# Optimization experiments

Measured on AMD Instinct MI355X. Metric: run time of the kernel, lower is better.

Reference implementation:

```python
import jax, jax.numpy as jnp
import numpy as np

K = 20          # neighbors per point (knn k=20)
BN_EPS = 1e-5   # torch BatchNorm1d default eps
NEG_SLOPE = 0.2 # LeakyReLU negative_slope


def setup_inputs() -> dict:
    key = jax.random.key(0)
    k1, k2 = jax.random.split(key)
    B, N, H = 8, 4096, 64
    pcd = jax.random.normal(k1, (B, N, 3), dtype=jnp.float32)
    W = jax.random.normal(k2, (6, H), dtype=jnp.float32) * (1.0 / np.sqrt(6.0))
    b = jnp.zeros((H,), dtype=jnp.float32)
    gamma = jnp.ones((H,), dtype=jnp.float32)
    beta = jnp.zeros((H,), dtype=jnp.float32)
    return {"pcd": pcd, "W": W, "b": b, "gamma": gamma, "beta": beta}


def reference(pcd, W, b, gamma, beta):
    # pcd: [B, N, 3]
    # --- kNN graph construction (per cloud, includes self like torch_geometric knn) ---
    sq = jnp.sum(pcd * pcd, axis=-1)                          # [B, N]
    # squared distances: |xi|^2 + |xj|^2 - 2 xi.xj  -> [B, N, N]
    d2 = sq[:, :, None] + sq[:, None, :] - 2.0 * jnp.einsum("bnd,bmd->bnm", pcd, pcd)
    _, idx = jax.lax.top_k(-d2, K)                            # idx: [B, N, K] neighbor indices

    # --- edge feature gather: concat(x_j, x_i - x_j) ---
    nbr = jax.vmap(lambda p, i: p[i])(pcd, idx)               # [B, N, K, 3]
    feat = jnp.concatenate([nbr, pcd[:, :, None, :] - nbr], axis=-1)  # [B, N, K, 6]

    # --- shared MLP: Linear(6,64) + BatchNorm1d(64, training stats) + LeakyReLU(0.2) ---
    h = jnp.einsum("bnkf,fh->bnkh", feat, W) + b              # [B, N, K, 64]
    mean = jnp.mean(h, axis=(0, 1, 2))
    var = jnp.mean((h - mean) ** 2, axis=(0, 1, 2))           # biased var (BN train mode)
    h = (h - mean) * jax.lax.rsqrt(var + BN_EPS) * gamma + beta
    h = jnp.where(h >= 0, h, NEG_SLOPE * h)

    # --- max-pool over the K edges of each point (max_pool_x per cluster) ---
    return jnp.max(h, axis=2)                                 # [B, N, 64]
```

## Files before the change

kernel.cpp:

```cpp
#include <hip/hip_runtime.h>
#include <math.h>

#define KNN 20
#define NPTS 4096
#define BATCH 8
#define P_TOT (BATCH * NPTS)
#define QPW 8
#define WPB 8
#define QPB (QPW * WPB)
#define NBLK (P_TOT / QPB)
#define BPB (NPTS / QPB)
#define BN_EPS 1e-5
#define NEG_SLOPE 0.2f

#define FO_CLOUD 0
#define FO_PART  131072
#define FO_PART2 196608
#define FO_AB    655360
#define FO_W2    655488
#define FO_BIG   655936

__global__ __launch_bounds__(256) void pack_kernel(const float* __restrict__ pcd,
                                                   float4* __restrict__ cloud) {
    int i = blockIdx.x * 256 + threadIdx.x;
    float x = pcd[3 * i], y = pcd[3 * i + 1], z = pcd[3 * i + 2];
    float sq = __fadd_rn(__fadd_rn(__fmul_rn(x, x), __fmul_rn(y, y)), __fmul_rn(z, z));
    cloud[i] = make_float4(x, y, z, sq);
}

#define DIST(C) ({ \
    float dot_ = __fadd_rn(__fadd_rn(__fmul_rn(qx, (C).x), __fmul_rn(qy, (C).y)), \
                           __fmul_rn(qz, (C).z)); \
    fmaf(-2.0f, dot_, __fadd_rn(qs, (C).w)); })

#define RECOMP(G) { \
    float m1 = INFINITY, m2 = INFINITY; int s1 = 0, s2 = 0; \
    _Pragma("unroll") \
    for (int e = 0; e < 8; ++e) { \
        const int sl = (G) * 8 + e; \
        const float4 C = cl[sl * 64 + lane]; \
        float dd = DIST(C); \
        if ((mask >> sl) & 1ull) dd = INFINITY; \
        if (dd < m1) { m2 = m1; s2 = s1; m1 = dd; s1 = sl; } \
        else if (dd < m2) { m2 = dd; s2 = sl; } \
    } \
    gv1[G] = m1; gs1[G] = s1; gv2[G] = m2; gs2[G] = s2; }

#define PROMOTE(G) { \
    if (gv2[G] < INFINITY) { gv1[G] = gv2[G]; gs1[G] = gs2[G]; gv2[G] = INFINITY; } \
    else { RECOMP(G) } }

template <bool FAST>
__global__ __launch_bounds__(512, 2) void knn_kernel(const float4* __restrict__ cloud,
                                                     const float* __restrict__ W,
                                                     const float* __restrict__ bias,
                                                     float* __restrict__ partials,
                                                     float* __restrict__ rawmax,
                                                     float* __restrict__ rawmin,
                                                     int* __restrict__ idxo) {
    __shared__ float4 cl[NPTS];
    const int t = threadIdx.x;
    const int wave = t >> 6, lane = t & 63;
    const int bidx = blockIdx.x;
    const int batch = bidx / BPB;
    const int gbase = batch * NPTS;

#pragma unroll
    for (int it = 0; it < NPTS / 512; ++it)
        cl[it * 512 + t] = cloud[gbase + it * 512 + t];
    __syncthreads();

    const float wc3 = W[192 + lane], wc4 = W[256 + lane], wc5 = W[320 + lane];
    const float wd0 = W[lane] - wc3, wd1 = W[64 + lane] - wc4, wd2 = W[128 + lane] - wc5;
    const float bb = bias[lane];
    float se = 0.f, sqs = 0.f;

#pragma unroll 1
    for (int qi = 0; qi < QPW; ++qi) {
        const int q = (bidx % BPB) * QPB + wave * QPW + qi;
        const int gq = gbase + q;
        const float4 Q = cl[q];
        const float qx = Q.x, qy = Q.y, qz = Q.z, qs = Q.w;
        const float qoff = fmaf(wc3, qx, fmaf(wc4, qy, fmaf(wc5, qz, bb)));

        float gv1[8], gv2[8];
        int gs1[8], gs2[8];
#pragma unroll
        for (int g = 0; g < 8; ++g) { gv1[g] = INFINITY; gv2[g] = INFINITY; gs1[g] = 0; gs2[g] = 0; }
#pragma unroll
        for (int g = 0; g < 8; ++g) {
#pragma unroll
            for (int e = 0; e < 8; ++e) {
                const int j = g * 8 + e;
                const float4 C = cl[j * 64 + lane];
                const float dd = DIST(C);
                const bool c1 = dd < gv1[g];
                const bool c2 = dd < gv2[g];
                gv2[g] = c1 ? gv1[g] : (c2 ? dd : gv2[g]);
                gs2[g] = c1 ? gs1[g] : (c2 ? j : gs2[g]);
                gv1[g] = c1 ? dd : gv1[g];
                gs1[g] = c1 ? j : gs1[g];
            }
            __builtin_amdgcn_sched_barrier(0);
        }
        float dmin = gv1[0]; int bs = gs1[0];
#pragma unroll
        for (int g = 1; g < 8; ++g) if (gv1[g] < dmin) { dmin = gv1[g]; bs = gs1[g]; }
        int mmin = bs * 64 + lane;
        unsigned long long mask = 0ull;
        float hmax = -INFINITY, hmin = INFINITY;

#pragma unroll 1
        for (int p = 0; p < KNN; ++p) {
            float gmin = dmin;
#pragma unroll
            for (int off = 32; off; off >>= 1) gmin = fminf(gmin, __shfl_xor(gmin, off));
            unsigned long long bal = __ballot(dmin == gmin);
            int win;
            if (__popcll(bal) > 1) {
                int mv = (dmin == gmin) ? mmin : 0x7FFFFFFF;
#pragma unroll
                for (int off = 32; off; off >>= 1) mv = min(mv, __shfl_xor(mv, off));
                win = mv;
            } else {
                win = __shfl(mmin, __ffsll((unsigned long long)bal) - 1);
            }

            if (!FAST) { if (lane == 0) idxo[gq * KNN + p] = win; }

            const float4 C = cl[win];
            const float raw = fmaf(wd0, C.x, fmaf(wd1, C.y, fmaf(wd2, C.z, qoff)));
            se += raw;
            sqs = fmaf(raw, raw, sqs);
            hmax = fmaxf(hmax, raw);
            hmin = fminf(hmin, raw);

            if ((win & 63) == lane) {
                const int slot = win >> 6;
                mask |= (1ull << slot);
                switch (slot >> 3) {
                    case 0: PROMOTE(0); break;
                    case 1: PROMOTE(1); break;
                    case 2: PROMOTE(2); break;
                    case 3: PROMOTE(3); break;
                    case 4: PROMOTE(4); break;
                    case 5: PROMOTE(5); break;
                    case 6: PROMOTE(6); break;
                    default: PROMOTE(7); break;
                }
                float nv = gv1[0]; int ns = gs1[0];
#pragma unroll
                for (int g2 = 1; g2 < 8; ++g2) if (gv1[g2] < nv) { nv = gv1[g2]; ns = gs1[g2]; }
                dmin = nv; mmin = ns * 64 + lane;
            }
        }

        if (FAST) {
            rawmax[gq * 64 + lane] = hmax;
            rawmin[gq * 64 + lane] = hmin;
        }
    }

    __syncthreads();
    float* sred = (float*)cl;
    sred[wave * 128 + lane] = se;
    sred[wave * 128 + 64 + lane] = sqs;
    __syncthreads();
    if (t < 128) {
        float s = 0.f;
#pragma unroll
        for (int w = 0; w < WPB; ++w) s += sred[w * 128 + t];
        partials[bidx * 128 + t] = s;
    }
}

__global__ __launch_bounds__(128) void finA_kernel(const float* __restrict__ partials,
                                                   float* __restrict__ part2) {
    const int b = blockIdx.x, t = threadIdx.x;
    float s = 0.f;
#pragma unroll
    for (int i = 0; i < 8; ++i) s += partials[(b * 8 + i) * 128 + t];
    part2[b * 128 + t] = s;
}

__global__ __launch_bounds__(64) void finB_kernel(const float* __restrict__ part2,
                                                  const float* __restrict__ W,
                                                  const float* __restrict__ bias,
                                                  const float* __restrict__ gamma,
                                                  const float* __restrict__ beta,
                                                  float* __restrict__ ab,
                                                  float* __restrict__ w2) {
    const int c = threadIdx.x;
    double s0 = 0.0, s1 = 0.0, q0 = 0.0, q1 = 0.0;
    for (int i = 0; i < 64; i += 2) {
        s0 += (double)part2[i * 128 + c];
        q0 += (double)part2[i * 128 + 64 + c];
        s1 += (double)part2[(i + 1) * 128 + c];
        q1 += (double)part2[(i + 1) * 128 + 64 + c];
    }
    const double cnt = (double)P_TOT * KNN;
    double mean = (s0 + s1) / cnt;
    double var = (q0 + q1) / cnt - mean * mean;
    double a = (double)gamma[c] / sqrt(var + BN_EPS);
    float af = (float)a;
    float sh = (float)((double)beta[c] - mean * a);
    ab[c] = af;
    ab[64 + c] = sh;
#pragma unroll
    for (int f = 0; f < 6; ++f) w2[f * 64 + c] = W[f * 64 + c] * af;
    w2[384 + c] = fmaf(bias[c], af, sh);
}

__global__ __launch_bounds__(256) void final_kernel(const float* __restrict__ ab,
                                                    const float* __restrict__ rawmin,
                                                    float* __restrict__ out) {
    int i = blockIdx.x * 256 + threadIdx.x;
    int c = i & 63;
    float a = ab[c], sh = ab[64 + c];
    float va = fmaf(a, out[i], sh);
    float vb = fmaf(a, rawmin[i], sh);
    va = va >= 0.f ? va : NEG_SLOPE * va;
    vb = vb >= 0.f ? vb : NEG_SLOPE * vb;
    out[i] = fmaxf(va, vb);
}

__global__ __launch_bounds__(256) void out_kernel(const float4* __restrict__ cloud,
                                                  const int* __restrict__ idxo,
                                                  const float* __restrict__ w2,
                                                  float* __restrict__ out) {
    const int t = threadIdx.x, c = t & 63;
    const int gp = blockIdx.x * 4 + (t >> 6);
    const int gb = gp & ~(NPTS - 1);
    const float wc0 = w2[c], wc1 = w2[64 + c], wc2 = w2[128 + c];
    const float wc3 = w2[192 + c], wc4 = w2[256 + c], wc5 = w2[320 + c];
    const float bc = w2[384 + c];
    const float4 Q = cloud[gp];
    float vmax = -INFINITY;
    for (int k = 0; k < KNN; ++k) {
        const int m = idxo[gp * KNN + k];
        const float4 C = cloud[gb + m];
        float h = bc;
        h = fmaf(wc0, C.x, h);
        h = fmaf(wc1, C.y, h);
        h = fmaf(wc2, C.z, h);
        h = fmaf(wc3, Q.x - C.x, h);
        h = fmaf(wc4, Q.y - C.y, h);
        h = fmaf(wc5, Q.z - C.z, h);
        h = h >= 0.f ? h : NEG_SLOPE * h;
        vmax = fmaxf(vmax, h);
    }
    out[gp * 64 + c] = vmax;
}

extern "C" void kernel_launch(void* const* d_in, const int* in_sizes, int n_in,
                              void* d_out, int out_size, void* d_ws, size_t ws_size,
                              hipStream_t stream) {
    const float* pcd   = (const float*)d_in[0];
    const float* W     = (const float*)d_in[1];
    const float* bias  = (const float*)d_in[2];
    const float* gamma = (const float*)d_in[3];
    const float* beta  = (const float*)d_in[4];

    float* wsf = (float*)d_ws;
    float4* cloud   = (float4*)(wsf + FO_CLOUD);
    float* partials = wsf + FO_PART;
    float* part2    = wsf + FO_PART2;
    float* ab       = wsf + FO_AB;
    float* w2       = wsf + FO_W2;
    float* big      = wsf + FO_BIG;
    float* out      = (float*)d_out;

    const size_t need_fast = (size_t)FO_BIG * 4 + (size_t)P_TOT * 64 * 4 + 1024;
    const bool fast = ws_size >= need_fast;

    pack_kernel<<<P_TOT / 256, 256, 0, stream>>>(pcd, cloud);
    if (fast) {
        knn_kernel<true><<<NBLK, 512, 0, stream>>>(cloud, W, bias, partials, out, big, nullptr);
        finA_kernel<<<64, 128, 0, stream>>>(partials, part2);
        finB_kernel<<<1, 64, 0, stream>>>(part2, W, bias, gamma, beta, ab, w2);
        final_kernel<<<(P_TOT * 64) / 256, 256, 0, stream>>>(ab, big, out);
    } else {
        knn_kernel<false><<<NBLK, 512, 0, stream>>>(cloud, W, bias, partials, nullptr, nullptr, (int*)big);
        finA_kernel<<<64, 128, 0, stream>>>(partials, part2);
        finB_kernel<<<1, 64, 0, stream>>>(part2, W, bias, gamma, beta, ab, w2);
        out_kernel<<<P_TOT / 4, 256, 0, stream>>>(cloud, (int*)big, w2, out);
    }
}
```

Baseline: 217.4 us.

## Process two queries per wave and use DPP/swizzle wave reductions in kNN

The kNN kernel now handles two query points per wave iteration, so each LDS load of a candidate point feeds two distance computations and the two 20-step selection loops are interleaved for more instruction-level parallelism. The shuffle-based wave min-reductions are replaced with ds_swizzle plus a single bpermute, and winner broadcast uses readlane. The cost is doubled per-query register state (32 extra candidate slots), which may raise VGPR pressure under the 512x2 launch bounds and risk spills.

```diff
diff --git a/kernel.cpp b/kernel.cpp
--- a/kernel.cpp
+++ b/kernel.cpp
@@ -28,27 +28,81 @@
     cloud[i] = make_float4(x, y, z, sq);
 }
 
-#define DIST(C) ({ \
-    float dot_ = __fadd_rn(__fadd_rn(__fmul_rn(qx, (C).x), __fmul_rn(qy, (C).y)), \
-                           __fmul_rn(qz, (C).z)); \
-    fmaf(-2.0f, dot_, __fadd_rn(qs, (C).w)); })
-
-#define RECOMP(G) { \
-    float m1 = INFINITY, m2 = INFINITY; int s1 = 0, s2 = 0; \
-    _Pragma("unroll") \
-    for (int e = 0; e < 8; ++e) { \
-        const int sl = (G) * 8 + e; \
-        const float4 C = cl[sl * 64 + lane]; \
-        float dd = DIST(C); \
-        if ((mask >> sl) & 1ull) dd = INFINITY; \
-        if (dd < m1) { m2 = m1; s2 = s1; m1 = dd; s1 = sl; } \
-        else if (dd < m2) { m2 = dd; s2 = sl; } \
-    } \
-    gv1[G] = m1; gs1[G] = s1; gv2[G] = m2; gs2[G] = s2; }
-
-#define PROMOTE(G) { \
-    if (gv2[G] < INFINITY) { gv1[G] = gv2[G]; gs1[G] = gs2[G]; gv2[G] = INFINITY; } \
-    else { RECOMP(G) } }
+__device__ __forceinline__ float distf(float4 C, float qx, float qy, float qz, float qs) {
+    float dot_ = __fadd_rn(__fadd_rn(__fmul_rn(qx, C.x), __fmul_rn(qy, C.y)),
+                           __fmul_rn(qz, C.z));
+    return fmaf(-2.0f, dot_, __fadd_rn(qs, C.w));
+}
+
+__device__ __forceinline__ void upd2(float& v1, float& v2, int& s1, int& s2, float dd, int j) {
+    const bool c1 = dd < v1;
+    const bool c2 = dd < v2;
+    v2 = c1 ? v1 : (c2 ? dd : v2);
+    s2 = c1 ? s1 : (c2 ? j : s2);
+    v1 = c1 ? dd : v1;
+    s1 = c1 ? j : s1;
+}
+
+__device__ __forceinline__ float wmin_f(float v, int a32) {
+    v = fminf(v, __int_as_float(__builtin_amdgcn_ds_swizzle(__float_as_int(v), 0x041F)));
+    v = fminf(v, __int_as_float(__builtin_amdgcn_ds_swizzle(__float_as_int(v), 0x081F)));
+    v = fminf(v, __int_as_float(__builtin_amdgcn_ds_swizzle(__float_as_int(v), 0x101F)));
+    v = fminf(v, __int_as_float(__builtin_amdgcn_ds_swizzle(__float_as_int(v), 0x201F)));
+    v = fminf(v, __int_as_float(__builtin_amdgcn_ds_swizzle(__float_as_int(v), 0x401F)));
+    v = fminf(v, __int_as_float(__builtin_amdgcn_ds_bpermute(a32, __float_as_int(v))));
+    return v;
+}
+__device__ __forceinline__ int wmin_i(int v, int a32) {
+    v = min(v, __builtin_amdgcn_ds_swizzle(v, 0x041F));
+    v = min(v, __builtin_amdgcn_ds_swizzle(v, 0x081F));
+    v = min(v, __builtin_amdgcn_ds_swizzle(v, 0x101F));
+    v = min(v, __builtin_amdgcn_ds_swizzle(v, 0x201F));
+    v = min(v, __builtin_amdgcn_ds_swizzle(v, 0x401F));
+    v = min(v, __builtin_amdgcn_ds_bpermute(a32, v));
+    return v;
+}
+
+template <int G>
+__device__ __forceinline__ void prom(float (&gv1)[8], float (&gv2)[8], int (&gs1)[8], int (&gs2)[8],
+                                     unsigned long long mask, const float4* cl, int lane,
+                                     float qx, float qy, float qz, float qs) {
+    if (gv2[G] < INFINITY) {
+        gv1[G] = gv2[G]; gs1[G] = gs2[G]; gv2[G] = INFINITY;
+    } else {
+        float m1 = INFINITY, m2 = INFINITY; int s1 = 0, s2 = 0;
+#pragma unroll
+        for (int e = 0; e < 8; ++e) {
+            const int sl = G * 8 + e;
+            const float4 C = cl[sl * 64 + lane];
+            float dd = distf(C, qx, qy, qz, qs);
+            if ((mask >> sl) & 1ull) dd = INFINITY;
+            upd2(m1, m2, s1, s2, dd, sl);
+        }
+        gv1[G] = m1; gv2[G] = m2; gs1[G] = s1; gs2[G] = s2;
+    }
+}
+
+__device__ __forceinline__ void repair(float (&gv1)[8], float (&gv2)[8], int (&gs1)[8], int (&gs2)[8],
+                                       unsigned long long& mask, float& dmin, int& mmin,
+                                       int win, int lane, const float4* cl,
+                                       float qx, float qy, float qz, float qs) {
+    const int slot = win >> 6;
+    mask |= (1ull << slot);
+    switch (slot >> 3) {
+        case 0: prom<0>(gv1, gv2, gs1, gs2, mask, cl, lane, qx, qy, qz, qs); break;
+        case 1: prom<1>(gv1, gv2, gs1, gs2, mask, cl, lane, qx, qy, qz, qs); break;
+        case 2: prom<2>(gv1, gv2, gs1, gs2, mask, cl, lane, qx, qy, qz, qs); break;
+        case 3: prom<3>(gv1, gv2, gs1, gs2, mask, cl, lane, qx, qy, qz, qs); break;
+        case 4: prom<4>(gv1, gv2, gs1, gs2, mask, cl, lane, qx, qy, qz, qs); break;
+        case 5: prom<5>(gv1, gv2, gs1, gs2, mask, cl, lane, qx, qy, qz, qs); break;
+        case 6: prom<6>(gv1, gv2, gs1, gs2, mask, cl, lane, qx, qy, qz, qs); break;
+        default: prom<7>(gv1, gv2, gs1, gs2, mask, cl, lane, qx, qy, qz, qs); break;
+    }
+    float nv = gv1[0]; int ns = gs1[0];
+#pragma unroll
+    for (int g = 1; g < 8; ++g) if (gv1[g] < nv) { nv = gv1[g]; ns = gs1[g]; }
+    dmin = nv; mmin = ns * 64 + lane;
+}
 
 template <bool FAST>
 __global__ __launch_bounds__(512, 2) void knn_kernel(const float4* __restrict__ cloud,
@@ -61,6 +115,7 @@
     __shared__ float4 cl[NPTS];
     const int t = threadIdx.x;
     const int wave = t >> 6, lane = t & 63;
+    const int a32 = ((lane ^ 32) << 2);
     const int bidx = blockIdx.x;
     const int batch = bidx / BPB;
     const int gbase = batch * NPTS;
@@ -76,88 +131,95 @@
     float se = 0.f, sqs = 0.f;
 
 #pragma unroll 1
-    for (int qi = 0; qi < QPW; ++qi) {
-        const int q = (bidx % BPB) * QPB + wave * QPW + qi;
-        const int gq = gbase + q;
-        const float4 Q = cl[q];
-        const float qx = Q.x, qy = Q.y, qz = Q.z, qs = Q.w;
-        const float qoff = fmaf(wc3, qx, fmaf(wc4, qy, fmaf(wc5, qz, bb)));
-
-        float gv1[8], gv2[8];
-        int gs1[8], gs2[8];
-#pragma unroll
-        for (int g = 0; g < 8; ++g) { gv1[g] = INFINITY; gv2[g] = INFINITY; gs1[g] = 0; gs2[g] = 0; }
+    for (int qi = 0; qi < QPW / 2; ++qi) {
+        const int qA = (bidx % BPB) * QPB + wave * QPW + qi * 2;
+        const int qB = qA + 1;
+        const int gqA = gbase + qA, gqB = gbase + qB;
+        const float4 QA = cl[qA];
+        const float4 QB = cl[qB];
+        const float qxA = QA.x, qyA = QA.y, qzA = QA.z, qsA = QA.w;
+        const float qxB = QB.x, qyB = QB.y, qzB = QB.z, qsB = QB.w;
+        const float qoffA = fmaf(wc3, qxA, fmaf(wc4, qyA, fmaf(wc5, qzA, bb)));
+        const float qoffB = fmaf(wc3, qxB, fmaf(wc4, qyB, fmaf(wc5, qzB, bb)));
+
+        float gv1A[8], gv2A[8], gv1B[8], gv2B[8];
+        int gs1A[8], gs2A[8], gs1B[8], gs2B[8];
+#pragma unroll
+        for (int g = 0; g < 8; ++g) {
+            gv1A[g] = INFINITY; gv2A[g] = INFINITY; gs1A[g] = 0; gs2A[g] = 0;
+            gv1B[g] = INFINITY; gv2B[g] = INFINITY; gs1B[g] = 0; gs2B[g] = 0;
+        }
 #pragma unroll
         for (int g = 0; g < 8; ++g) {
 #pragma unroll
             for (int e = 0; e < 8; ++e) {
                 const int j = g * 8 + e;
                 const float4 C = cl[j * 64 + lane];
-                const float dd = DIST(C);
-                const bool c1 = dd < gv1[g];
-                const bool c2 = dd < gv2[g];
-                gv2[g] = c1 ? gv1[g] : (c2 ? dd : gv2[g]);
-                gs2[g] = c1 ? gs1[g] : (c2 ? j : gs2[g]);
-                gv1[g] = c1 ? dd : gv1[g];
-                gs1[g] = c1 ? j : gs1[g];
+                const float ddA = distf(C, qxA, qyA, qzA, qsA);
+                const float ddB = distf(C, qxB, qyB, qzB, qsB);
+                upd2(gv1A[g], gv2A[g], gs1A[g], gs2A[g], ddA, j);
+                upd2(gv1B[g], gv2B[g], gs1B[g], gs2B[g], ddB, j);
             }
             __builtin_amdgcn_sched_barrier(0);
         }
-        float dmin = gv1[0]; int bs = gs1[0];
-#pragma unroll
-        for (int g = 1; g < 8; ++g) if (gv1[g] < dmin) { dmin = gv1[g]; bs = gs1[g]; }
-        int mmin = bs * 64 + lane;
-        unsigned long long mask = 0ull;
-        float hmax = -INFINITY, hmin = INFINITY;
+        float dminA = gv1A[0]; int bsA = gs1A[0];
+        float dminB = gv1B[0]; int bsB = gs1B[0];
+#pragma unroll
+        for (int g = 1; g < 8; ++g) {
+            if (gv1A[g] < dminA) { dminA = gv1A[g]; bsA = gs1A[g]; }
+            if (gv1B[g] < dminB) { dminB = gv1B[g]; bsB = gs1B[g]; }
+        }
+        int mminA = bsA * 64 + lane;
+        int mminB = bsB * 64 + lane;
+        unsigned long long maskA = 0ull, maskB = 0ull;
+        float hmaxA = -INFINITY, hminA = INFINITY;
+        float hmaxB = -INFINITY, hminB = INFINITY;
 
 #pragma unroll 1
         for (int p = 0; p < KNN; ++p) {
-            float gmin = dmin;
-#pragma unroll
-            for (int off = 32; off; off >>= 1) gmin = fminf(gmin, __shfl_xor(gmin, off));
-            unsigned long long bal = __ballot(dmin == gmin);
-            int win;
-            if (__popcll(bal) > 1) {
-                int mv = (dmin == gmin) ? mmin : 0x7FFFFFFF;
-#pragma unroll
-                for (int off = 32; off; off >>= 1) mv = min(mv, __shfl_xor(mv, off));
-                win = mv;
+            const float gA = wmin_f(dminA, a32);
+            const float gB = wmin_f(dminB, a32);
+            const unsigned long long balA = __ballot(dminA == gA);
+            const unsigned long long balB = __ballot(dminB == gB);
+            int winA, winB;
+            if (__builtin_expect(__popcll(balA) > 1, 0)) {
+                winA = wmin_i((dminA == gA) ? mminA : 0x7FFFFFFF, a32);
             } else {
-                win = __shfl(mmin, __ffsll((unsigned long long)bal) - 1);
+                winA = __builtin_amdgcn_readlane(mminA, (int)(__ffsll(balA) - 1));
             }
-
-            if (!FAST) { if (lane == 0) idxo[gq * KNN + p] = win; }
-
-            const float4 C = cl[win];
-            const float raw = fmaf(wd0, C.x, fmaf(wd1, C.y, fmaf(wd2, C.z, qoff)));
-            se += raw;
-            sqs = fmaf(raw, raw, sqs);
-            hmax = fmaxf(hmax, raw);
-            hmin = fminf(hmin, raw);
-
-            if ((win & 63) == lane) {
-                const int slot = win >> 6;
-                mask |= (1ull << slot);
-                switch (slot >> 3) {
-                    case 0: PROMOTE(0); break;
-                    case 1: PROMOTE(1); break;
-                    case 2: PROMOTE(2); break;
-                    case 3: PROMOTE(3); break;
-                    case 4: PROMOTE(4); break;
-                    case 5: PROMOTE(5); break;
-                    case 6: PROMOTE(6); break;
-                    default: PROMOTE(7); break;
+            if (__builtin_expect(__popcll(balB) > 1, 0)) {
+                winB = wmin_i((dminB == gB) ? mminB : 0x7FFFFFFF, a32);
+            } else {
+                winB = __builtin_amdgcn_readlane(mminB, (int)(__ffsll(balB) - 1));
+            }
+
+            if (!FAST) {
+                if (lane == 0) {
+                    idxo[gqA * KNN + p] = winA;
+                    idxo[gqB * KNN + p] = winB;
                 }
-                float nv = gv1[0]; int ns = gs1[0];
-#pragma unroll
-                for (int g2 = 1; g2 < 8; ++g2) if (gv1[g2] < nv) { nv = gv1[g2]; ns = gs1[g2]; }
-                dmin = nv; mmin = ns * 64 + lane;
             }
+
+            const float4 CA = cl[winA];
+            const float4 CB = cl[winB];
+            const float rawA = fmaf(wd0, CA.x, fmaf(wd1, CA.y, fmaf(wd2, CA.z, qoffA)));
+            const float rawB = fmaf(wd0, CB.x, fmaf(wd1, CB.y, fmaf(wd2, CB.z, qoffB)));
+            se += rawA; sqs = fmaf(rawA, rawA, sqs);
+            hmaxA = fmaxf(hmaxA, rawA); hminA = fminf(hminA, rawA);
+            se += rawB; sqs = fmaf(rawB, rawB, sqs);
+            hmaxB = fmaxf(hmaxB, rawB); hminB = fminf(hminB, rawB);
+
+            if ((winA & 63) == lane)
+                repair(gv1A, gv2A, gs1A, gs2A, maskA, dminA, mminA, winA, lane, cl, qxA, qyA, qzA, qsA);
+            if ((winB & 63) == lane)
+                repair(gv1B, gv2B, gs1B, gs2B, maskB, dminB, mminB, winB, lane, cl, qxB, qyB, qzB, qsB);
         }
 
         if (FAST) {
-            rawmax[gq * 64 + lane] = hmax;
-            rawmin[gq * 64 + lane] = hmin;
+            rawmax[gqA * 64 + lane] = hmaxA;
+            rawmin[gqA * 64 + lane] = hminA;
+            rawmax[gqB * 64 + lane] = hmaxB;
+            rawmin[gqB * 64 + lane] = hminB;
         }
     }
 
```

Result: slower. 271.8 us (+25.0%).
